# Kernel optimization log

Measured on AMD Instinct MI355X. Metric: run time of the kernel, lower is better.

Reference implementation:

```python
import jax, jax.numpy as jnp
import numpy as np

DIS_NORM = 6.0 * 512 / 1000.0  # 6 * D(z=0) * Nmesh / Boxsize with D(0)=1


def setup_inputs() -> dict:
    key = jax.random.key(0)
    x = jax.random.normal(key, (2, 4, 128, 128, 128), dtype=jnp.float32)
    return {"x": x}


def _lag2eul(x):
    N, C = x.shape[0], x.shape[1]
    D, H, W = x.shape[2], x.shape[3], x.shape[4]
    P = D * H * W
    Cout = C - 3 if C > 3 else 1

    # rm_dis_mean=True: mean displacement, detached
    dis_mean = jax.lax.stop_gradient(jnp.mean(x[:, :3], axis=(2, 3, 4), keepdims=True))

    pos = (x[:, :3] - dis_mean) * DIS_NORM  # (N,3,D,H,W)
    gd = jnp.arange(D, dtype=x.dtype) + 0.5
    gh = jnp.arange(H, dtype=x.dtype) + 0.5
    gw = jnp.arange(W, dtype=x.dtype) + 0.5
    grid = jnp.stack(jnp.meshgrid(gd, gh, gw, indexing='ij'))  # (3,D,H,W)
    pos = (pos + grid[None]).reshape(N, 3, P)

    if C > 3:
        val = x[:, 3:].reshape(N, Cout, P)
    else:
        val = jnp.ones((N, Cout, P), dtype=x.dtype)

    intpos = jnp.floor(pos).astype(jnp.int32)
    # 8 trilinear neighbors: bit b of n -> offset along dim b
    neighbors = (jnp.arange(8, dtype=jnp.int32)[None, :] >> jnp.arange(3, dtype=jnp.int32)[:, None]) & 1  # (3,8)
    tgt = intpos[:, :, :, None] + neighbors[None, :, None, :]  # (N,3,P,8)

    kernel = jnp.prod(1.0 - jnp.abs(pos[:, :, :, None] - tgt.astype(x.dtype)), axis=1)  # (N,P,8)
    src = val[:, :, :, None] * kernel[:, None, :, :]  # (N,Cout,P,8)

    # periodic=False: mask out-of-bounds deposits
    bounds = jnp.array([D, H, W], dtype=jnp.int32)[None, :, None, None]
    mask = jnp.all((tgt >= 0) & (tgt < bounds), axis=1)  # (N,P,8)
    ind = (tgt[:, 0] * H + tgt[:, 1]) * W + tgt[:, 2]  # (N,P,8)
    ind = jnp.clip(ind, 0, P - 1)
    src = jnp.where(mask[:, None, :, :], src, jnp.zeros((), dtype=x.dtype))

    def scatter_one(ind_n, src_n):
        mesh = jnp.zeros((Cout, P), dtype=src_n.dtype)
        return mesh.at[:, ind_n.reshape(-1)].add(src_n.reshape(Cout, -1))

    mesh = jax.vmap(scatter_one)(ind, src)  # (N,Cout,P)
    return mesh.reshape(N, Cout, D, H, W)


def reference(x):
    return _lag2eul(x)
```

## Files before the change

### kernel.cpp

```cpp
#include <hip/hip_runtime.h>

#define NBATCH 2
#define NDIM   128
#define NP     (128 * 128 * 128)
#define DIS_NORM 3.072f

#define TS   16
#define LO   5
#define HI   6
#define WIN  (TS + LO + HI)
#define WIN2 (WIN * WIN)
#define WINF (WIN * WIN * WIN)
#define SLOT 19684
#define TPB  8
#define NTILE (TPB * TPB * TPB)

#define FXSCALE 16777216.0f
#define FXINV   (1.0f / 16777216.0f)

#define SUMS_OFF 0
#define WINS_OFF 1024
#define WS_FLOATS ((size_t)WINS_OFF + (size_t)NBATCH * NTILE * SLOT)
#define WS_NEEDED_BYTES (WS_FLOATS * sizeof(float))

__global__ __launch_bounds__(256) void prep_kernel(const float* __restrict__ x,
                                                   float* __restrict__ ws,
                                                   float* __restrict__ out) {
    const int plane = blockIdx.y;
    if (plane < 6) {
        const int n = plane / 3, c = plane % 3;
        const float4* xp = (const float4*)(x + ((size_t)n * 4 + c) * NP);
        const int nvec = NP / 4;
        float s = 0.0f;
        for (int i = blockIdx.x * 256 + threadIdx.x; i < nvec; i += 128 * 256) {
            float4 v = xp[i];
            s += (v.x + v.y) + (v.z + v.w);
        }
        #pragma unroll
        for (int off = 32; off > 0; off >>= 1) s += __shfl_down(s, off, 64);
        __shared__ float wsum[4];
        if ((threadIdx.x & 63) == 0) wsum[threadIdx.x >> 6] = s;
        __syncthreads();
        if (threadIdx.x == 0)
            ws[SUMS_OFF + plane * 128 + blockIdx.x] =
                (wsum[0] + wsum[1]) + (wsum[2] + wsum[3]);
    } else {
        float4* o4 = (float4*)out;
        const int nvec = NBATCH * NP / 4;
        const float4 z = make_float4(0.f, 0.f, 0.f, 0.f);
        for (int i = blockIdx.x * 256 + threadIdx.x; i < nvec; i += 128 * 256)
            o4[i] = z;
    }
}

__device__ __forceinline__ void load_means(const float* __restrict__ ws, int n,
                                           float& m0, float& m1, float& m2) {
    float s0 = 0.f, s1 = 0.f, s2 = 0.f;
    const float* p0 = ws + SUMS_OFF + (n * 3 + 0) * 128;
    const float* p1 = ws + SUMS_OFF + (n * 3 + 1) * 128;
    const float* p2 = ws + SUMS_OFF + (n * 3 + 2) * 128;
    #pragma unroll 4
    for (int b = 0; b < 128; ++b) { s0 += p0[b]; s1 += p1[b]; s2 += p2[b]; }
    const float inv_np = 1.0f / (float)NP;
    m0 = s0 * inv_np; m1 = s1 * inv_np; m2 = s2 * inv_np;
}

__device__ __forceinline__ void deposit_pair(unsigned long long* __restrict__ winU,
                                             int b, float va, float vb) {
    const int fa = __float2int_rn(va * FXSCALE);
    const int fb = __float2int_rn(vb * FXSCALE);
    const bool odd = (b & 1);
    const long long packed = (((long long)fb) << 32) + (long long)fa;
    const long long hiOnly = ((long long)fa) << 32;
    atomicAdd(&winU[b >> 1], (unsigned long long)(odd ? hiOnly : packed));
    if (odd) atomicAdd(&winU[(b >> 1) + 1], (unsigned long long)(long long)fb);
}

__global__ __launch_bounds__(512, 4) void scatter_tile_kernel(
        const float* __restrict__ x, const float* __restrict__ ws,
        float* __restrict__ wins, float* __restrict__ out) {
    const int blk = blockIdx.x;
    const int n = blk >> 9;
    const int t = blk & (NTILE - 1);
    const int tx = t & 7, ty = (t >> 3) & 7, tz = t >> 6;

    __shared__ ulonglong2 win2[SLOT / 4];
    unsigned long long* winU = (unsigned long long*)win2;
    {
        float4* z4 = (float4*)win2;
        const float4 z = make_float4(0.f, 0.f, 0.f, 0.f);
        for (int i = threadIdx.x; i < SLOT / 4; i += 512) z4[i] = z;
    }

    float m0, m1, m2;
    load_means(ws, n, m0, m1, m2);
    __syncthreads();

    const int i0 = threadIdx.x * 8;
    const int lw0 = i0 & 15;
    const int lh  = (i0 >> 4) & 15;
    const int ld  = i0 >> 8;
    const int gd = tz * TS + ld, gh = ty * TS + lh, gw0 = tx * TS + lw0;
    const size_t prow = ((size_t)gd * NDIM + gh) * NDIM + gw0;

    const float4* x4 = (const float4*)(x + (size_t)n * 4 * NP);
    const size_t q = prow >> 2;
    const size_t s4 = NP / 4;
    float4 a0 = x4[0 * s4 + q], a1 = x4[0 * s4 + q + 1];
    float4 b0 = x4[1 * s4 + q], b1 = x4[1 * s4 + q + 1];
    float4 c0 = x4[2 * s4 + q], c1 = x4[2 * s4 + q + 1];
    float4 e0 = x4[3 * s4 + q], e1 = x4[3 * s4 + q + 1];
    const float D0[8] = {a0.x, a0.y, a0.z, a0.w, a1.x, a1.y, a1.z, a1.w};
    const float D1[8] = {b0.x, b0.y, b0.z, b0.w, b1.x, b1.y, b1.z, b1.w};
    const float D2[8] = {c0.x, c0.y, c0.z, c0.w, c1.x, c1.y, c1.z, c1.w};
    const float VV[8] = {e0.x, e0.y, e0.z, e0.w, e1.x, e1.y, e1.z, e1.w};

    const int od = tz * TS - LO, oh = ty * TS - LO, ow = tx * TS - LO;
    float* sp = out + (size_t)n * NP;

    #pragma unroll
    for (int k = 0; k < 8; ++k) {
        const float pd = (D0[k] - m0) * DIS_NORM + (float)gd + 0.5f;
        const float ph = (D1[k] - m1) * DIS_NORM + (float)gh + 0.5f;
        const float pw = (D2[k] - m2) * DIS_NORM + (float)(gw0 + k) + 0.5f;
        const float v = VV[k];

        const float fd = floorf(pd), fh = floorf(ph), fw = floorf(pw);
        const int id = (int)fd, ih = (int)fh, iw = (int)fw;
        const float rd = pd - fd, rh = ph - fh, rw = pw - fw;

        const int wd = id - od, wh = ih - oh, ww = iw - ow;
        if ((unsigned)wd <= WIN - 2 && (unsigned)wh <= WIN - 2 &&
            (unsigned)ww <= WIN - 2) {
            const int b00 = (wd * WIN + wh) * WIN + ww;
            const float sd0 = v * (1.0f - rd), sd1 = v * rd;
            const float h0 = 1.0f - rh, h1 = rh;
            const float q0 = 1.0f - rw, q1 = rw;
            deposit_pair(winU, b00,               sd0 * h0 * q0, sd0 * h0 * q1);
            deposit_pair(winU, b00 + WIN,         sd0 * h1 * q0, sd0 * h1 * q1);
            deposit_pair(winU, b00 + WIN2,        sd1 * h0 * q0, sd1 * h0 * q1);
            deposit_pair(winU, b00 + WIN2 + WIN,  sd1 * h1 * q0, sd1 * h1 * q1);
        } else {
            const float wd2[2]  = {1.0f - rd, rd};
            const float wh2[2]  = {1.0f - rh, rh};
            const float ww2[2]  = {1.0f - rw, rw};
            #pragma unroll
            for (int dd = 0; dd < 2; ++dd) {
                const int td = id + dd, wdc = wd + dd;
                const bool dW = (unsigned)wdc < WIN, dM = (unsigned)td < NDIM;
                if (!dM && !dW) continue;
                #pragma unroll
                for (int hh = 0; hh < 2; ++hh) {
                    const int th = ih + hh, whc = wh + hh;
                    const bool hW = (unsigned)whc < WIN, hM = (unsigned)th < NDIM;
                    const float vdh = v * wd2[dd] * wh2[hh];
                    #pragma unroll
                    for (int wi = 0; wi < 2; ++wi) {
                        const int tw = iw + wi, wwc = ww + wi;
                        const bool wW = (unsigned)wwc < WIN, wM = (unsigned)tw < NDIM;
                        const float dep = vdh * ww2[wi];
                        if (dW && hW && wW) {
                            const int cb = (wdc * WIN + whc) * WIN + wwc;
                            const int fx = __float2int_rn(dep * FXSCALE);
                            const long long cv = (cb & 1)
                                ? (((long long)fx) << 32) : (long long)fx;
                            atomicAdd(&winU[cb >> 1], (unsigned long long)cv);
                        } else if (dM && hM && wM) {
                            atomicAdd(sp + ((size_t)td * NDIM + th) * NDIM + tw, dep);
                        }
                    }
                }
            }
        }
    }

    __syncthreads();
    float4* dst = (float4*)(wins + (size_t)blk * SLOT);
    for (int i = threadIdx.x; i < SLOT / 4; i += 512) {
        const ulonglong2 tv = win2[i];
        const int a0i = (int)(unsigned)(tv.x & 0xffffffffull);
        const int b0i = (int)(tv.x >> 32) + (a0i < 0 ? 1 : 0);
        const int a1i = (int)(unsigned)(tv.y & 0xffffffffull);
        const int b1i = (int)(tv.y >> 32) + (a1i < 0 ? 1 : 0);
        dst[i] = make_float4((float)a0i * FXINV, (float)b0i * FXINV,
                             (float)a1i * FXINV, (float)b1i * FXINV);
    }
}

__device__ __forceinline__ int axis_tiles(int c, int* t, int* l) {
    const int r = c & (TS - 1), t0 = c >> 4;
    int cnt = 0;
    t[cnt] = t0; l[cnt] = r + LO; cnt++;
    if (r < HI && t0 > 0)            { t[cnt] = t0 - 1; l[cnt] = r + TS + LO; cnt++; }
    if (r >= TS - LO && t0 < TPB - 1){ t[cnt] = t0 + 1; l[cnt] = r - (TS - LO); cnt++; }
    return cnt;
}

__global__ __launch_bounds__(256) void gather_kernel(const float* __restrict__ wins,
                                                     float* __restrict__ out) {
    const size_t i4 = (size_t)blockIdx.x * 256 + threadIdx.x;
    const int n = (int)(i4 >> 19);
    const int p = (int)((i4 & ((NP / 4) - 1)) << 2);
    const int w0 = p & 127, h = (p >> 7) & 127, d = p >> 14;

    float4 acc = ((const float4*)out)[i4];
    float* accf = (float*)&acc;

    int tzv[2], lzv[2], tyv[2], lyv[2], txv[2], lxv[2];
    const int nz = axis_tiles(d, tzv, lzv);
    const int ny = axis_tiles(h, tyv, lyv);

    for (int j = 0; j < 4; ++j) {
        const int nx = axis_tiles(w0 + j, txv, lxv);
        float a = 0.f;
        for (int za = 0; za < nz; ++za) {
            for (int ya = 0; ya < ny; ++ya) {
                const int tbase = n * NTILE + tzv[za] * 64 + tyv[ya] * 8;
                const int lbase = (lzv[za] * WIN + lyv[ya]) * WIN;
                for (int xa = 0; xa < nx; ++xa)
                    a += wins[(size_t)(tbase + txv[xa]) * SLOT + lbase + lxv[xa]];
            }
        }
        accf[j] += a;
    }
    ((float4*)out)[i4] = acc;
}

__global__ __launch_bounds__(256) void scatter_direct_kernel(const float* __restrict__ x,
                                                             const float* __restrict__ ws,
                                                             float* __restrict__ out) {
    const int lin = blockIdx.x * 256 + threadIdx.x;
    const int n = lin >> 21;
    const int p = lin & (NP - 1);

    float m0, m1, m2;
    load_means(ws, n, m0, m1, m2);

    const size_t base = (size_t)n * 4 * NP;
    const float d0 = x[base + 0 * (size_t)NP + p];
    const float d1 = x[base + 1 * (size_t)NP + p];
    const float d2 = x[base + 2 * (size_t)NP + p];
    const float v  = x[base + 3 * (size_t)NP + p];

    const int w = p & 127, h = (p >> 7) & 127, d = p >> 14;
    const float pd = (d0 - m0) * DIS_NORM + (float)d + 0.5f;
    const float ph = (d1 - m1) * DIS_NORM + (float)h + 0.5f;
    const float pw = (d2 - m2) * DIS_NORM + (float)w + 0.5f;
    const float fd = floorf(pd), fh = floorf(ph), fw = floorf(pw);
    const int id = (int)fd, ih = (int)fh, iw = (int)fw;
    const float rd = pd - fd, rh = ph - fh, rw = pw - fw;
    const float wd[2] = {1.0f - rd, rd}, wh[2] = {1.0f - rh, rh}, ww[2] = {1.0f - rw, rw};
    float* o = out + (size_t)n * NP;
    #pragma unroll
    for (int dd = 0; dd < 2; ++dd) {
        const int td = id + dd;
        if ((unsigned)td >= (unsigned)NDIM) continue;
        #pragma unroll
        for (int hh = 0; hh < 2; ++hh) {
            const int th = ih + hh;
            if ((unsigned)th >= (unsigned)NDIM) continue;
            const float vdh = v * wd[dd] * wh[hh];
            const int rowbase = (td * NDIM + th) * NDIM;
            #pragma unroll
            for (int wi = 0; wi < 2; ++wi) {
                const int tw = iw + wi;
                if ((unsigned)tw >= (unsigned)NDIM) continue;
                atomicAdd(o + rowbase + tw, vdh * ww[wi]);
            }
        }
    }
}

extern "C" void kernel_launch(void* const* d_in, const int* in_sizes, int n_in,
                              void* d_out, int out_size, void* d_ws, size_t ws_size,
                              hipStream_t stream) {
    const float* x = (const float*)d_in[0];
    float* out = (float*)d_out;
    float* ws = (float*)d_ws;
    float* wins = ws + WINS_OFF;

    dim3 pgrid(128, 7);

    if (ws_size >= WS_NEEDED_BYTES) {
        prep_kernel<<<pgrid, 256, 0, stream>>>(x, ws, out);
        scatter_tile_kernel<<<dim3(NBATCH * NTILE), 512, 0, stream>>>(
            x, ws, wins, out);
        gather_kernel<<<dim3(NBATCH * NP / 4 / 256), 256, 0, stream>>>(wins, out);
    } else {
        prep_kernel<<<pgrid, 256, 0, stream>>>(x, ws, out);
        scatter_direct_kernel<<<dim3(NBATCH * NP / 256), 256, 0, stream>>>(x, ws, out);
    }
}
```

Before: 199.7 us.

## Fuse prep, scatter and gather into one cooperative kernel with grid syncs

The three kernel launches (mean reduction plus output zeroing, tiled shared-memory scatter, gather) are merged into one cooperative kernel of 512 blocks that separates the phases with grid.sync(). Each block reduces partial sums, recomputes the means after the first sync, then scatters its tile for both batches in turn. The aim is to remove launch gaps and tail effects between kernels. In exchange each block does twice the scatter work serially, all 512 blocks must be co-resident (four per CU), and grid-wide barriers add cost. A fallback to the old three-kernel path runs if the cooperative launch fails.

New measurement: 339.1 us. 1.7x slower.

```diff
diff --git a/kernel.cpp b/kernel.cpp
--- a/kernel.cpp
+++ b/kernel.cpp
@@ -1,4 +1,7 @@
 #include <hip/hip_runtime.h>
+#include <hip/hip_cooperative_groups.h>
+
+namespace cg = cooperative_groups;
 
 #define NBATCH 2
 #define NDIM   128
@@ -18,52 +21,14 @@
 #define FXSCALE 16777216.0f
 #define FXINV   (1.0f / 16777216.0f)
 
+#define NBLK 512
+#define NTHR 512
+
 #define SUMS_OFF 0
-#define WINS_OFF 1024
+#define WINS_OFF 4096
 #define WS_FLOATS ((size_t)WINS_OFF + (size_t)NBATCH * NTILE * SLOT)
 #define WS_NEEDED_BYTES (WS_FLOATS * sizeof(float))
 
-__global__ __launch_bounds__(256) void prep_kernel(const float* __restrict__ x,
-                                                   float* __restrict__ ws,
-                                                   float* __restrict__ out) {
-    const int plane = blockIdx.y;
-    if (plane < 6) {
-        const int n = plane / 3, c = plane % 3;
-        const float4* xp = (const float4*)(x + ((size_t)n * 4 + c) * NP);
-        const int nvec = NP / 4;
-        float s = 0.0f;
-        for (int i = blockIdx.x * 256 + threadIdx.x; i < nvec; i += 128 * 256) {
-            float4 v = xp[i];
-            s += (v.x + v.y) + (v.z + v.w);
-        }
-        #pragma unroll
-        for (int off = 32; off > 0; off >>= 1) s += __shfl_down(s, off, 64);
-        __shared__ float wsum[4];
-        if ((threadIdx.x & 63) == 0) wsum[threadIdx.x >> 6] = s;
-        __syncthreads();
-        if (threadIdx.x == 0)
-            ws[SUMS_OFF + plane * 128 + blockIdx.x] =
-                (wsum[0] + wsum[1]) + (wsum[2] + wsum[3]);
-    } else {
-        float4* o4 = (float4*)out;
-        const int nvec = NBATCH * NP / 4;
-        const float4 z = make_float4(0.f, 0.f, 0.f, 0.f);
-        for (int i = blockIdx.x * 256 + threadIdx.x; i < nvec; i += 128 * 256)
-            o4[i] = z;
-    }
-}
-
-__device__ __forceinline__ void load_means(const float* __restrict__ ws, int n,
-                                           float& m0, float& m1, float& m2) {
-    float s0 = 0.f, s1 = 0.f, s2 = 0.f;
-    const float* p0 = ws + SUMS_OFF + (n * 3 + 0) * 128;
-    const float* p1 = ws + SUMS_OFF + (n * 3 + 1) * 128;
-    const float* p2 = ws + SUMS_OFF + (n * 3 + 2) * 128;
-    #pragma unroll 4
-    for (int b = 0; b < 128; ++b) { s0 += p0[b]; s1 += p1[b]; s2 += p2[b]; }
-    const float inv_np = 1.0f / (float)NP;
-    m0 = s0 * inv_np; m1 = s1 * inv_np; m2 = s2 * inv_np;
-}
 
 __device__ __forceinline__ void deposit_pair(unsigned long long* __restrict__ winU,
                                              int b, float va, float vb) {
@@ -76,25 +41,12 @@
     if (odd) atomicAdd(&winU[(b >> 1) + 1], (unsigned long long)(long long)fb);
 }
 
-__global__ __launch_bounds__(512, 4) void scatter_tile_kernel(
-        const float* __restrict__ x, const float* __restrict__ ws,
+__device__ __forceinline__ void scatter_tile_body(
+        const float* __restrict__ x, float m0, float m1, float m2,
+        int n, int t, ulonglong2* __restrict__ win2,
         float* __restrict__ wins, float* __restrict__ out) {
-    const int blk = blockIdx.x;
-    const int n = blk >> 9;
-    const int t = blk & (NTILE - 1);
+    unsigned long long* winU = (unsigned long long*)win2;
     const int tx = t & 7, ty = (t >> 3) & 7, tz = t >> 6;
-
-    __shared__ ulonglong2 win2[SLOT / 4];
-    unsigned long long* winU = (unsigned long long*)win2;
-    {
-        float4* z4 = (float4*)win2;
-        const float4 z = make_float4(0.f, 0.f, 0.f, 0.f);
-        for (int i = threadIdx.x; i < SLOT / 4; i += 512) z4[i] = z;
-    }
-
-    float m0, m1, m2;
-    load_means(ws, n, m0, m1, m2);
-    __syncthreads();
 
     const int i0 = threadIdx.x * 8;
     const int lw0 = i0 & 15;
@@ -136,10 +88,10 @@
             const float sd0 = v * (1.0f - rd), sd1 = v * rd;
             const float h0 = 1.0f - rh, h1 = rh;
             const float q0 = 1.0f - rw, q1 = rw;
-            deposit_pair(winU, b00,               sd0 * h0 * q0, sd0 * h0 * q1);
-            deposit_pair(winU, b00 + WIN,         sd0 * h1 * q0, sd0 * h1 * q1);
-            deposit_pair(winU, b00 + WIN2,        sd1 * h0 * q0, sd1 * h0 * q1);
-            deposit_pair(winU, b00 + WIN2 + WIN,  sd1 * h1 * q0, sd1 * h1 * q1);
+            deposit_pair(winU, b00,              sd0 * h0 * q0, sd0 * h0 * q1);
+            deposit_pair(winU, b00 + WIN,        sd0 * h1 * q0, sd0 * h1 * q1);
+            deposit_pair(winU, b00 + WIN2,       sd1 * h0 * q0, sd1 * h0 * q1);
+            deposit_pair(winU, b00 + WIN2 + WIN, sd1 * h1 * q0, sd1 * h1 * q1);
         } else {
             const float wd2[2]  = {1.0f - rd, rd};
             const float wh2[2]  = {1.0f - rh, rh};
@@ -175,8 +127,8 @@
     }
 
     __syncthreads();
-    float4* dst = (float4*)(wins + (size_t)blk * SLOT);
-    for (int i = threadIdx.x; i < SLOT / 4; i += 512) {
+    float4* dst = (float4*)(wins + (size_t)((n << 9) | t) * SLOT);
+    for (int i = threadIdx.x; i < SLOT / 4; i += NTHR) {
         const ulonglong2 tv = win2[i];
         const int a0i = (int)(unsigned)(tv.x & 0xffffffffull);
         const int b0i = (int)(tv.x >> 32) + (a0i < 0 ? 1 : 0);
@@ -196,9 +148,8 @@
     return cnt;
 }
 
-__global__ __launch_bounds__(256) void gather_kernel(const float* __restrict__ wins,
-                                                     float* __restrict__ out) {
-    const size_t i4 = (size_t)blockIdx.x * 256 + threadIdx.x;
+__device__ __forceinline__ void gather_cells(const float* __restrict__ wins,
+                                             float* __restrict__ out, size_t i4) {
     const int n = (int)(i4 >> 19);
     const int p = (int)((i4 & ((NP / 4) - 1)) << 2);
     const int w0 = p & 127, h = (p >> 7) & 127, d = p >> 14;
@@ -226,6 +177,149 @@
     ((float4*)out)[i4] = acc;
 }
 
+__global__ __launch_bounds__(NTHR, 4) void fused_kernel(const float* __restrict__ x,
+                                                        float* __restrict__ ws,
+                                                        float* __restrict__ wins,
+                                                        float* __restrict__ out) {
+    cg::grid_group grid = cg::this_grid();
+    const int blk = blockIdx.x;
+
+    __shared__ ulonglong2 win2[SLOT / 4];
+    __shared__ float wsum[8];
+    __shared__ float meansh[6];
+
+    {
+        float4* o4 = (float4*)out;
+        const float4 z = make_float4(0.f, 0.f, 0.f, 0.f);
+        for (int i = blk * NTHR + threadIdx.x; i < NBATCH * NP / 4; i += NBLK * NTHR)
+            o4[i] = z;
+    }
+    for (int plane = 0; plane < 6; ++plane) {
+        const int n = plane / 3, c = plane % 3;
+        const float4* xp = (const float4*)(x + ((size_t)n * 4 + c) * NP);
+        float s = 0.0f;
+        for (int i = blk * NTHR + threadIdx.x; i < NP / 4; i += NBLK * NTHR) {
+            float4 v = xp[i];
+            s += (v.x + v.y) + (v.z + v.w);
+        }
+        #pragma unroll
+        for (int off = 32; off > 0; off >>= 1) s += __shfl_down(s, off, 64);
+        if ((threadIdx.x & 63) == 0) wsum[threadIdx.x >> 6] = s;
+        __syncthreads();
+        if (threadIdx.x == 0) {
+            float tt = 0.f;
+            #pragma unroll
+            for (int j = 0; j < 8; ++j) tt += wsum[j];
+            ws[SUMS_OFF + plane * NBLK + blk] = tt;
+        }
+        __syncthreads();
+    }
+    grid.sync();
+
+    {
+        const float inv_np = 1.0f / (float)NP;
+        for (int plane = 0; plane < 6; ++plane) {
+            float s = ws[SUMS_OFF + plane * NBLK + threadIdx.x];
+            #pragma unroll
+            for (int off = 32; off > 0; off >>= 1) s += __shfl_down(s, off, 64);
+            if ((threadIdx.x & 63) == 0) wsum[threadIdx.x >> 6] = s;
+            __syncthreads();
+            if (threadIdx.x == 0) {
+                float tt = 0.f;
+                #pragma unroll
+                for (int j = 0; j < 8; ++j) tt += wsum[j];
+                meansh[plane] = tt * inv_np;
+            }
+            __syncthreads();
+        }
+    }
+    const float mn0 = meansh[0], mn1 = meansh[1], mn2 = meansh[2];
+    const float mn3 = meansh[3], mn4 = meansh[4], mn5 = meansh[5];
+
+    #pragma unroll
+    for (int nb = 0; nb < NBATCH; ++nb) {
+        {
+            float4* z4 = (float4*)win2;
+            const float4 z = make_float4(0.f, 0.f, 0.f, 0.f);
+            for (int i = threadIdx.x; i < SLOT / 4; i += NTHR) z4[i] = z;
+        }
+        __syncthreads();
+        if (nb == 0) scatter_tile_body(x, mn0, mn1, mn2, 0, blk, win2, wins, out);
+        else         scatter_tile_body(x, mn3, mn4, mn5, 1, blk, win2, wins, out);
+        __syncthreads();
+    }
+    grid.sync();
+
+    for (size_t i4 = (size_t)blk * NTHR + threadIdx.x; i4 < (size_t)NBATCH * NP / 4;
+         i4 += (size_t)NBLK * NTHR)
+        gather_cells(wins, out, i4);
+}
+
+__global__ __launch_bounds__(256) void prep_kernel(const float* __restrict__ x,
+                                                   float* __restrict__ ws,
+                                                   float* __restrict__ out) {
+    const int plane = blockIdx.y;
+    if (plane < 6) {
+        const int n = plane / 3, c = plane % 3;
+        const float4* xp = (const float4*)(x + ((size_t)n * 4 + c) * NP);
+        float s = 0.0f;
+        for (int i = blockIdx.x * 256 + threadIdx.x; i < NP / 4; i += 128 * 256) {
+            float4 v = xp[i];
+            s += (v.x + v.y) + (v.z + v.w);
+        }
+        #pragma unroll
+        for (int off = 32; off > 0; off >>= 1) s += __shfl_down(s, off, 64);
+        __shared__ float wsum[4];
+        if ((threadIdx.x & 63) == 0) wsum[threadIdx.x >> 6] = s;
+        __syncthreads();
+        if (threadIdx.x == 0)
+            ws[SUMS_OFF + plane * 128 + blockIdx.x] =
+                (wsum[0] + wsum[1]) + (wsum[2] + wsum[3]);
+    } else {
+        float4* o4 = (float4*)out;
+        const float4 z = make_float4(0.f, 0.f, 0.f, 0.f);
+        for (int i = blockIdx.x * 256 + threadIdx.x; i < NBATCH * NP / 4; i += 128 * 256)
+            o4[i] = z;
+    }
+}
+
+__device__ __forceinline__ void load_means128(const float* __restrict__ ws, int n,
+                                              float& m0, float& m1, float& m2) {
+    float s0 = 0.f, s1 = 0.f, s2 = 0.f;
+    const float* p0 = ws + SUMS_OFF + (n * 3 + 0) * 128;
+    const float* p1 = ws + SUMS_OFF + (n * 3 + 1) * 128;
+    const float* p2 = ws + SUMS_OFF + (n * 3 + 2) * 128;
+    #pragma unroll 4
+    for (int b = 0; b < 128; ++b) { s0 += p0[b]; s1 += p1[b]; s2 += p2[b]; }
+    const float inv_np = 1.0f / (float)NP;
+    m0 = s0 * inv_np; m1 = s1 * inv_np; m2 = s2 * inv_np;
+}
+
+__global__ __launch_bounds__(NTHR, 4) void scatter_tile_kernel(
+        const float* __restrict__ x, const float* __restrict__ ws,
+        float* __restrict__ wins, float* __restrict__ out) {
+    const int blk = blockIdx.x;
+    const int n = blk >> 9;
+    const int t = blk & (NTILE - 1);
+
+    __shared__ ulonglong2 win2[SLOT / 4];
+    {
+        float4* z4 = (float4*)win2;
+        const float4 z = make_float4(0.f, 0.f, 0.f, 0.f);
+        for (int i = threadIdx.x; i < SLOT / 4; i += NTHR) z4[i] = z;
+    }
+    float m0, m1, m2;
+    load_means128(ws, n, m0, m1, m2);
+    __syncthreads();
+    scatter_tile_body(x, m0, m1, m2, n, t, win2, wins, out);
+}
+
+__global__ __launch_bounds__(256) void gather_kernel(const float* __restrict__ wins,
+                                                     float* __restrict__ out) {
+    const size_t i4 = (size_t)blockIdx.x * 256 + threadIdx.x;
+    gather_cells(wins, out, i4);
+}
+
 __global__ __launch_bounds__(256) void scatter_direct_kernel(const float* __restrict__ x,
                                                              const float* __restrict__ ws,
                                                              float* __restrict__ out) {
@@ -234,7 +328,7 @@
     const int p = lin & (NP - 1);
 
     float m0, m1, m2;
-    load_means(ws, n, m0, m1, m2);
+    load_means128(ws, n, m0, m1, m2);
 
     const size_t base = (size_t)n * 4 * NP;
     const float d0 = x[base + 0 * (size_t)NP + p];
@@ -279,14 +373,19 @@
     float* ws = (float*)d_ws;
     float* wins = ws + WINS_OFF;
 
-    dim3 pgrid(128, 7);
-
     if (ws_size >= WS_NEEDED_BYTES) {
+        void* args[4] = {(void*)&x, (void*)&ws, (void*)&wins, (void*)&out};
+        hipError_t e = hipLaunchCooperativeKernel((const void*)fused_kernel,
+                                                  dim3(NBLK), dim3(NTHR),
+                                                  args, 0, stream);
+        if (e == hipSuccess) return;
+        (void)hipGetLastError();
+        dim3 pgrid(128, 7);
         prep_kernel<<<pgrid, 256, 0, stream>>>(x, ws, out);
-        scatter_tile_kernel<<<dim3(NBATCH * NTILE), 512, 0, stream>>>(
-            x, ws, wins, out);
+        scatter_tile_kernel<<<dim3(NBATCH * NTILE), NTHR, 0, stream>>>(x, ws, wins, out);
         gather_kernel<<<dim3(NBATCH * NP / 4 / 256), 256, 0, stream>>>(wins, out);
     } else {
+        dim3 pgrid(128, 7);
         prep_kernel<<<pgrid, 256, 0, stream>>>(x, ws, out);
         scatter_direct_kernel<<<dim3(NBATCH * NP / 256), 256, 0, stream>>>(x, ws, out);
     }
```

## Route tile window halos into destination-tile slabs and gather per tile in shared memory

Applied to the files above, without the earlier changes.

The scatter kernel no longer writes its whole window as one slot. It splits the window into 27 sections and writes each section into a slab owned by the destination tile, so each tile's incoming contributions sit contiguously. A new per-tile gather kernel sums the up-to-27 sections into a shared-memory 16^3 tile and adds it to the output with coalesced float4 accesses. This replaces the per-point gather, which did scattered reads across neighbouring windows. The cost is scattered, less coalesced global writes in the scatter epilogue and 27 synchronized passes in the gather.

Result: slower. 214.8 us (+7.6%).

```diff
diff --git a/kernel.cpp b/kernel.cpp
--- a/kernel.cpp
+++ b/kernel.cpp
@@ -11,16 +11,18 @@
 #define WIN  (TS + LO + HI)
 #define WIN2 (WIN * WIN)
 #define WINF (WIN * WIN * WIN)
-#define SLOT 19684
 #define TPB  8
 #define NTILE (TPB * TPB * TPB)
+#define NTHR 512
 
 #define FXSCALE 16777216.0f
 #define FXINV   (1.0f / 16777216.0f)
 
+#define SLAB 19696
+
 #define SUMS_OFF 0
-#define WINS_OFF 1024
-#define WS_FLOATS ((size_t)WINS_OFF + (size_t)NBATCH * NTILE * SLOT)
+#define SLABS_OFF 1024
+#define WS_FLOATS ((size_t)SLABS_OFF + (size_t)NBATCH * NTILE * SLAB)
 #define WS_NEEDED_BYTES (WS_FLOATS * sizeof(float))
 
 __global__ __launch_bounds__(256) void prep_kernel(const float* __restrict__ x,
@@ -30,9 +32,8 @@
     if (plane < 6) {
         const int n = plane / 3, c = plane % 3;
         const float4* xp = (const float4*)(x + ((size_t)n * 4 + c) * NP);
-        const int nvec = NP / 4;
         float s = 0.0f;
-        for (int i = blockIdx.x * 256 + threadIdx.x; i < nvec; i += 128 * 256) {
+        for (int i = blockIdx.x * 256 + threadIdx.x; i < NP / 4; i += 128 * 256) {
             float4 v = xp[i];
             s += (v.x + v.y) + (v.z + v.w);
         }
@@ -46,15 +47,14 @@
                 (wsum[0] + wsum[1]) + (wsum[2] + wsum[3]);
     } else {
         float4* o4 = (float4*)out;
-        const int nvec = NBATCH * NP / 4;
         const float4 z = make_float4(0.f, 0.f, 0.f, 0.f);
-        for (int i = blockIdx.x * 256 + threadIdx.x; i < nvec; i += 128 * 256)
+        for (int i = blockIdx.x * 256 + threadIdx.x; i < NBATCH * NP / 4; i += 128 * 256)
             o4[i] = z;
     }
 }
 
-__device__ __forceinline__ void load_means(const float* __restrict__ ws, int n,
-                                           float& m0, float& m1, float& m2) {
+__device__ __forceinline__ void load_means128(const float* __restrict__ ws, int n,
+                                              float& m0, float& m1, float& m2) {
     float s0 = 0.f, s1 = 0.f, s2 = 0.f;
     const float* p0 = ws + SUMS_OFF + (n * 3 + 0) * 128;
     const float* p1 = ws + SUMS_OFF + (n * 3 + 1) * 128;
@@ -76,24 +76,23 @@
     if (odd) atomicAdd(&winU[(b >> 1) + 1], (unsigned long long)(long long)fb);
 }
 
-__global__ __launch_bounds__(512, 4) void scatter_tile_kernel(
+__global__ __launch_bounds__(NTHR, 4) void scatter_tile_kernel(
         const float* __restrict__ x, const float* __restrict__ ws,
-        float* __restrict__ wins, float* __restrict__ out) {
+        float* __restrict__ slabs, float* __restrict__ out) {
     const int blk = blockIdx.x;
     const int n = blk >> 9;
     const int t = blk & (NTILE - 1);
     const int tx = t & 7, ty = (t >> 3) & 7, tz = t >> 6;
 
-    __shared__ ulonglong2 win2[SLOT / 4];
+    __shared__ ulonglong2 win2[(WINF + 3) / 4 + 1];
     unsigned long long* winU = (unsigned long long*)win2;
     {
         float4* z4 = (float4*)win2;
         const float4 z = make_float4(0.f, 0.f, 0.f, 0.f);
-        for (int i = threadIdx.x; i < SLOT / 4; i += 512) z4[i] = z;
-    }
-
+        for (int i = threadIdx.x; i < (WINF + 3) / 4 + 1; i += NTHR) z4[i] = z;
+    }
     float m0, m1, m2;
-    load_means(ws, n, m0, m1, m2);
+    load_means128(ws, n, m0, m1, m2);
     __syncthreads();
 
     const int i0 = threadIdx.x * 8;
@@ -136,10 +135,10 @@
             const float sd0 = v * (1.0f - rd), sd1 = v * rd;
             const float h0 = 1.0f - rh, h1 = rh;
             const float q0 = 1.0f - rw, q1 = rw;
-            deposit_pair(winU, b00,               sd0 * h0 * q0, sd0 * h0 * q1);
-            deposit_pair(winU, b00 + WIN,         sd0 * h1 * q0, sd0 * h1 * q1);
-            deposit_pair(winU, b00 + WIN2,        sd1 * h0 * q0, sd1 * h0 * q1);
-            deposit_pair(winU, b00 + WIN2 + WIN,  sd1 * h1 * q0, sd1 * h1 * q1);
+            deposit_pair(winU, b00,              sd0 * h0 * q0, sd0 * h0 * q1);
+            deposit_pair(winU, b00 + WIN,        sd0 * h1 * q0, sd0 * h1 * q1);
+            deposit_pair(winU, b00 + WIN2,       sd1 * h0 * q0, sd1 * h0 * q1);
+            deposit_pair(winU, b00 + WIN2 + WIN, sd1 * h1 * q0, sd1 * h1 * q1);
         } else {
             const float wd2[2]  = {1.0f - rd, rd};
             const float wh2[2]  = {1.0f - rh, rh};
@@ -175,55 +174,98 @@
     }
 
     __syncthreads();
-    float4* dst = (float4*)(wins + (size_t)blk * SLOT);
-    for (int i = threadIdx.x; i < SLOT / 4; i += 512) {
-        const ulonglong2 tv = win2[i];
-        const int a0i = (int)(unsigned)(tv.x & 0xffffffffull);
-        const int b0i = (int)(tv.x >> 32) + (a0i < 0 ? 1 : 0);
-        const int a1i = (int)(unsigned)(tv.y & 0xffffffffull);
-        const int b1i = (int)(tv.y >> 32) + (a1i < 0 ? 1 : 0);
-        dst[i] = make_float4((float)a0i * FXINV, (float)b0i * FXINV,
-                             (float)a1i * FXINV, (float)b1i * FXINV);
-    }
-}
-
-__device__ __forceinline__ int axis_tiles(int c, int* t, int* l) {
-    const int r = c & (TS - 1), t0 = c >> 4;
-    int cnt = 0;
-    t[cnt] = t0; l[cnt] = r + LO; cnt++;
-    if (r < HI && t0 > 0)            { t[cnt] = t0 - 1; l[cnt] = r + TS + LO; cnt++; }
-    if (r >= TS - LO && t0 < TPB - 1){ t[cnt] = t0 + 1; l[cnt] = r - (TS - LO); cnt++; }
-    return cnt;
-}
-
-__global__ __launch_bounds__(256) void gather_kernel(const float* __restrict__ wins,
-                                                     float* __restrict__ out) {
-    const size_t i4 = (size_t)blockIdx.x * 256 + threadIdx.x;
-    const int n = (int)(i4 >> 19);
-    const int p = (int)((i4 & ((NP / 4) - 1)) << 2);
-    const int w0 = p & 127, h = (p >> 7) & 127, d = p >> 14;
-
-    float4 acc = ((const float4*)out)[i4];
-    float* accf = (float*)&acc;
-
-    int tzv[2], lzv[2], tyv[2], lyv[2], txv[2], lxv[2];
-    const int nz = axis_tiles(d, tzv, lzv);
-    const int ny = axis_tiles(h, tyv, lyv);
-
-    for (int j = 0; j < 4; ++j) {
-        const int nx = axis_tiles(w0 + j, txv, lxv);
-        float a = 0.f;
-        for (int za = 0; za < nz; ++za) {
-            for (int ya = 0; ya < ny; ++ya) {
-                const int tbase = n * NTILE + tzv[za] * 64 + tyv[ya] * 8;
-                const int lbase = (lzv[za] * WIN + lyv[ya]) * WIN;
-                for (int xa = 0; xa < nx; ++xa)
-                    a += wins[(size_t)(tbase + txv[xa]) * SLOT + lbase + lxv[xa]];
+
+    const int EXT[3]  = {6, 16, 5};
+    const int BASE[27] = {0,216,792,972,1548,3084,3564,3744,4224,
+                          4376,4952,6488,6968,8504,12600,13880,14360,15640,
+                          16040,16220,16700,16852,17332,18612,19012,19164,19564};
+    const int nbase = n << 9;
+
+    for (int c = threadIdx.x; c < WINF; c += NTHR) {
+        const int lz = c / WIN2;
+        const int rz = c - lz * WIN2;
+        const int ly = rz / WIN;
+        const int lx = rz - ly * WIN;
+
+        int mz, pz;
+        if (lz < LO) { mz = -1; pz = lz; }
+        else if (lz < LO + TS) { mz = 0; pz = lz - LO; }
+        else { mz = 1; pz = lz - LO - TS; }
+        int my, py;
+        if (ly < LO) { my = -1; py = ly; }
+        else if (ly < LO + TS) { my = 0; py = ly - LO; }
+        else { my = 1; py = ly - LO - TS; }
+        int mx, px;
+        if (lx < LO) { mx = -1; px = lx; }
+        else if (lx < LO + TS) { mx = 0; px = lx - LO; }
+        else { mx = 1; px = lx - LO - TS; }
+
+        const int dtz = tz + mz, dty = ty + my, dtx = tx + mx;
+        if ((unsigned)dtz >= TPB || (unsigned)dty >= TPB || (unsigned)dtx >= TPB)
+            continue;
+
+        const int jz = 1 - mz, jy = 1 - my, jx = 1 - mx;
+        const int po = jz * 9 + jy * 3 + jx;
+        const int linear = (pz * EXT[jy] + py) * EXT[jx] + px;
+
+        const unsigned long long u = winU[c >> 1];
+        const int lo = (int)(unsigned)(u & 0xffffffffull);
+        const int hi = (int)(u >> 32) + (lo < 0 ? 1 : 0);
+        const float val = (float)((c & 1) ? hi : lo) * FXINV;
+
+        slabs[(size_t)(nbase + (dtz * 8 + dty) * 8 + dtx) * SLAB + BASE[po] + linear] = val;
+    }
+}
+
+__global__ __launch_bounds__(NTHR) void gather_tile_kernel(const float* __restrict__ slabs,
+                                                           float* __restrict__ out) {
+    const int blk = blockIdx.x;
+    const int t = blk & (NTILE - 1);
+    const int tx = t & 7, ty = (t >> 3) & 7, tz = t >> 6;
+
+    __shared__ float tile[TS * TS * TS];
+    for (int i = threadIdx.x; i < TS * TS * TS; i += NTHR) tile[i] = 0.0f;
+    __syncthreads();
+
+    const float* slab = slabs + (size_t)blk * SLAB;
+    const int EXT[3] = {6, 16, 5};
+    const int DST[3] = {0, 0, 11};
+    const int BASE[27] = {0,216,792,972,1548,3084,3564,3744,4224,
+                          4376,4952,6488,6968,8504,12600,13880,14360,15640,
+                          16040,16220,16700,16852,17332,18612,19012,19164,19564};
+
+    #pragma unroll
+    for (int sec = 0; sec < 27; ++sec) {
+        const int jz = sec / 9, jy = (sec / 3) % 3, jx = sec % 3;
+        const int oz = jz - 1, oy = jy - 1, ox = jx - 1;
+        if ((unsigned)(tz + oz) < TPB && (unsigned)(ty + oy) < TPB &&
+            (unsigned)(tx + ox) < TPB) {
+            const int ez = EXT[jz], ey = EXT[jy], ex = EXT[jx];
+            const int npc = ez * ey * ex;
+            const int sz = DST[jz], sy = DST[jy], sx = DST[jx];
+            const float* pc = slab + BASE[sec];
+            for (int i = threadIdx.x; i < npc; i += NTHR) {
+                const int pz = i / (ey * ex);
+                const int r  = i - pz * (ey * ex);
+                const int py = r / ex;
+                const int px = r - py * ex;
+                tile[((sz + pz) * TS + sy + py) * TS + sx + px] += pc[i];
             }
         }
-        accf[j] += a;
-    }
-    ((float4*)out)[i4] = acc;
+        __syncthreads();
+    }
+
+    const int n = blk >> 9;
+    float* ob = out + (size_t)n * NP;
+    for (int i4 = threadIdx.x; i4 < TS * TS * TS / 4; i4 += NTHR) {
+        const int xq = i4 & 3, y = (i4 >> 2) & 15, z = i4 >> 6;
+        float4 v = ((const float4*)tile)[i4];
+        const size_t g = (((size_t)(tz * TS + z) * NDIM) + ty * TS + y) * NDIM
+                       + tx * TS + xq * 4;
+        float4 o = *(const float4*)(ob + g);
+        v.x += o.x; v.y += o.y; v.z += o.z; v.w += o.w;
+        *(float4*)(ob + g) = v;
+    }
 }
 
 __global__ __launch_bounds__(256) void scatter_direct_kernel(const float* __restrict__ x,
@@ -234,7 +276,7 @@
     const int p = lin & (NP - 1);
 
     float m0, m1, m2;
-    load_means(ws, n, m0, m1, m2);
+    load_means128(ws, n, m0, m1, m2);
 
     const size_t base = (size_t)n * 4 * NP;
     const float d0 = x[base + 0 * (size_t)NP + p];
@@ -277,15 +319,14 @@
     const float* x = (const float*)d_in[0];
     float* out = (float*)d_out;
     float* ws = (float*)d_ws;
-    float* wins = ws + WINS_OFF;
+    float* slabs = ws + SLABS_OFF;
 
     dim3 pgrid(128, 7);
 
     if (ws_size >= WS_NEEDED_BYTES) {
         prep_kernel<<<pgrid, 256, 0, stream>>>(x, ws, out);
-        scatter_tile_kernel<<<dim3(NBATCH * NTILE), 512, 0, stream>>>(
-            x, ws, wins, out);
-        gather_kernel<<<dim3(NBATCH * NP / 4 / 256), 256, 0, stream>>>(wins, out);
+        scatter_tile_kernel<<<dim3(NBATCH * NTILE), NTHR, 0, stream>>>(x, ws, slabs, out);
+        gather_tile_kernel<<<dim3(NBATCH * NTILE), NTHR, 0, stream>>>(slabs, out);
     } else {
         prep_kernel<<<pgrid, 256, 0, stream>>>(x, ws, out);
         scatter_direct_kernel<<<dim3(NBATCH * NP / 256), 256, 0, stream>>>(x, ws, out);
```
